# Optimization experiments

Hardware: AMD Instinct MI355X
Metric: run time of the kernel (lower is better)

The kernel has to match this reference:

```python
import jax, jax.numpy as jnp
import numpy as np

N, FIN = 4096, 128
HEADS = [8, 1]
FEATS = [64, 64]
NEG_SLOPE = 0.2
EDGE_P = 0.01  # edge density for the synthetic graph


def _init_w(key, shape, fan_in, fan_out):
    # VarianceScaling(1.0, 'fan_avg', 'uniform')
    limit = jnp.sqrt(3.0 / ((fan_in + fan_out) / 2.0))
    return jax.random.uniform(key, shape, jnp.float32, -limit, limit)


def setup_inputs() -> dict:
    key = jax.random.key(0)
    ks = jax.random.split(key, 12)
    x = jax.random.normal(ks[0], (N, FIN), jnp.float32)
    # additive connectivity mask: 0 on edges (incl. self-loops), -1e9 elsewhere
    adj = jax.random.bernoulli(ks[1], EDGE_P, (N, N))
    adj = adj | jnp.eye(N, dtype=bool)
    mask = jnp.where(adj, 0.0, -1e9).astype(jnp.float32)

    fin0, out0 = FIN, HEADS[0] * FEATS[0]
    fin1, out1 = out0, HEADS[1] * FEATS[1]
    W0 = _init_w(ks[2], (fin0, out0), fin0, out0)
    b0 = jnp.zeros((out0,), jnp.float32)
    a_src0 = _init_w(ks[3], (1, HEADS[0], FEATS[0]), 1, HEADS[0] * FEATS[0])
    a_tgt0 = _init_w(ks[4], (1, HEADS[0], FEATS[0]), 1, HEADS[0] * FEATS[0])
    W1 = _init_w(ks[5], (fin1, out1), fin1, out1)
    b1 = jnp.zeros((out1,), jnp.float32)
    a_src1 = _init_w(ks[6], (1, HEADS[1], FEATS[1]), 1, HEADS[1] * FEATS[1])
    a_tgt1 = _init_w(ks[7], (1, HEADS[1], FEATS[1]), 1, HEADS[1] * FEATS[1])
    return {
        "node_features": x, "connectivity_mask": mask,
        "W0": W0, "b0": b0, "a_src0": a_src0, "a_tgt0": a_tgt0,
        "W1": W1, "b1": b1, "a_src1": a_src1, "a_tgt1": a_tgt1,
    }


def _gat_layer(x, mask, W, b, a_src, a_tgt, num_heads, num_features):
    # (N, FIN) @ (FIN, H*F) -> (N, H, F)
    proj = (x @ W + b).reshape(-1, num_heads, num_features)
    s_src = jnp.sum(proj * a_src, axis=-1)  # (N, H)
    s_tgt = jnp.sum(proj * a_tgt, axis=-1)  # (N, H)
    # (H, N, 1) + (H, 1, N) -> (H, N, N)
    scores = s_src.T[:, :, None] + s_tgt.T[:, None, :]
    scores = jax.nn.leaky_relu(scores, negative_slope=NEG_SLOPE)
    att = jax.nn.softmax(scores + mask[None, :, :], axis=-1)  # (H, N, N)
    out = jnp.einsum('hnm,mhf->nhf', att, proj)  # (N, H, F)
    return out.reshape(-1, num_heads * num_features)


def reference(node_features, connectivity_mask, W0, b0, a_src0, a_tgt0,
              W1, b1, a_src1, a_tgt1):
    h = _gat_layer(node_features, connectivity_mask, W0, b0, a_src0, a_tgt0,
                   HEADS[0], FEATS[0])
    h = _gat_layer(h, connectivity_mask, W1, b1, a_src1, a_tgt1,
                   HEADS[1], FEATS[1])
    return h  # (N, HEADS[1]*FEATS[1])
```

## Files before the change

### kernel.cpp

```cpp
#include <hip/hip_runtime.h>
#include <hip/hip_bf16.h>

#define NNODES 4096
#define CAP 256


__global__ __launch_bounds__(256) void phase1_kernel(
    const float* __restrict__ mask, int* __restrict__ deg,
    unsigned short* __restrict__ cols, const float* __restrict__ x,
    const float* __restrict__ W0, const float* __restrict__ b0,
    const float* __restrict__ a_src0, const float* __restrict__ a_tgt0,
    const float* __restrict__ W1, float* __restrict__ Ph,
    float* __restrict__ ssrc0, float* __restrict__ stgt0) {
  __shared__ float smem[6144];
  const int t = threadIdx.x;
  if (blockIdx.x >= 1024) {
    const int n = blockIdx.x - 1024;
    const int lane = t & 63, wid = t >> 6;
    int* wsum = (int*)smem;
    const float4* row = (const float4*)(mask + (size_t)n * NNODES);
    float4 v[4];
    int cnt = 0;
#pragma unroll
    for (int j = 0; j < 4; ++j) {
      v[j] = row[t + 256 * j];
      cnt += (v[j].x == 0.0f) + (v[j].y == 0.0f) + (v[j].z == 0.0f) +
             (v[j].w == 0.0f);
    }
    int xs = cnt;
#pragma unroll
    for (int o = 1; o < 64; o <<= 1) {
      int y = __shfl_up(xs, o);
      if (lane >= o) xs += y;
    }
    if (lane == 63) wsum[wid] = xs;
    __syncthreads();
    int base = 0;
    for (int w = 0; w < wid; ++w) base += wsum[w];
    int off = base + xs - cnt;
    if (t == 0) {
      int total = wsum[0] + wsum[1] + wsum[2] + wsum[3];
      deg[n] = total < CAP ? total : CAP;
    }
    unsigned short* dst = cols + (size_t)n * CAP;
#pragma unroll
    for (int j = 0; j < 4; ++j) {
      const int c0 = (t + 256 * j) * 4;
      float fv[4] = {v[j].x, v[j].y, v[j].z, v[j].w};
#pragma unroll
      for (int k = 0; k < 4; ++k) {
        if (fv[k] == 0.0f) {
          if (off < CAP) dst[off] = (unsigned short)(c0 + k);
          ++off;
        }
      }
    }
  } else {
    float(*As)[36] = (float(*)[36])smem;
    float(*Ws)[64] = (float(*)[64])(smem + 1152);
    const int bx = blockIdx.x;
    const int brow = (bx & 127) * 32;
    const int head = bx >> 7;
    const int bcol = head * 64;
    const int tx = t & 15, ty = t >> 4;
    const int ar = t >> 3, ak = (t & 7) * 4;
    float acc[2][4] = {};
    for (int c = 0; c < 4; ++c) {
      const int k0 = c * 32;
      *(float4*)&As[ar][ak] =
          *(const float4*)&x[(size_t)(brow + ar) * 128 + k0 + ak];
#pragma unroll
      for (int q = 0; q < 2; ++q) {
        int i = t + q * 256;
        int k = i >> 4, c4 = (i & 15) * 4;
        *(float4*)&Ws[k][c4] =
            *(const float4*)&W0[(size_t)(k0 + k) * 512 + bcol + c4];
      }
      __syncthreads();
#pragma unroll 2
      for (int kk = 0; kk < 32; kk += 4) {
        float4 a0 = *(const float4*)&As[ty * 2 + 0][kk];
        float4 a1 = *(const float4*)&As[ty * 2 + 1][kk];
#pragma unroll
        for (int j = 0; j < 4; ++j) {
          float4 w = *(const float4*)&Ws[kk + j][tx * 4];
          float av0 = ((const float*)&a0)[j];
          float av1 = ((const float*)&a1)[j];
          acc[0][0] = fmaf(av0, w.x, acc[0][0]);
          acc[0][1] = fmaf(av0, w.y, acc[0][1]);
          acc[0][2] = fmaf(av0, w.z, acc[0][2]);
          acc[0][3] = fmaf(av0, w.w, acc[0][3]);
          acc[1][0] = fmaf(av1, w.x, acc[1][0]);
          acc[1][1] = fmaf(av1, w.y, acc[1][1]);
          acc[1][2] = fmaf(av1, w.z, acc[1][2]);
          acc[1][3] = fmaf(av1, w.w, acc[1][3]);
        }
      }
      __syncthreads();
    }
    float(*tile)[64] = (float(*)[64])smem;
    float(*W1s)[64] = (float(*)[64])(smem + 2048);
    const float4 bv = *(const float4*)&b0[bcol + tx * 4];
    const float4 as = *(const float4*)&a_src0[head * 64 + tx * 4];
    const float4 at = *(const float4*)&a_tgt0[head * 64 + tx * 4];
#pragma unroll
    for (int r = 0; r < 2; ++r) {
      float4 o;
      o.x = acc[r][0] + bv.x; o.y = acc[r][1] + bv.y;
      o.z = acc[r][2] + bv.z; o.w = acc[r][3] + bv.w;
      const int rowl = ty * 2 + r;
      *(float4*)&tile[rowl][tx * 4] = o;
      float ps = o.x * as.x + o.y * as.y + o.z * as.z + o.w * as.w;
      float pt = o.x * at.x + o.y * at.y + o.z * at.z + o.w * at.w;
#pragma unroll
      for (int m = 8; m; m >>= 1) {
        ps += __shfl_xor(ps, m);
        pt += __shfl_xor(pt, m);
      }
      if (tx == 0) {
        const size_t node = brow + rowl;
        ssrc0[node * 8 + head] = ps;
        stgt0[node * 8 + head] = pt;
      }
    }
    for (int i = t; i < 1024; i += 256) {
      const int k = i >> 4, c4 = (i & 15) * 4;
      *(float4*)&W1s[k][c4] =
          *(const float4*)&W1[(size_t)(head * 64 + k) * 64 + c4];
    }
    __syncthreads();
    float acc2[2][4] = {};
#pragma unroll 4
    for (int k = 0; k < 64; ++k) {
      const float4 w4 = *(const float4*)&W1s[k][tx * 4];
      const float a0 = tile[ty * 2 + 0][k];
      const float a1 = tile[ty * 2 + 1][k];
      acc2[0][0] = fmaf(a0, w4.x, acc2[0][0]);
      acc2[0][1] = fmaf(a0, w4.y, acc2[0][1]);
      acc2[0][2] = fmaf(a0, w4.z, acc2[0][2]);
      acc2[0][3] = fmaf(a0, w4.w, acc2[0][3]);
      acc2[1][0] = fmaf(a1, w4.x, acc2[1][0]);
      acc2[1][1] = fmaf(a1, w4.y, acc2[1][1]);
      acc2[1][2] = fmaf(a1, w4.z, acc2[1][2]);
      acc2[1][3] = fmaf(a1, w4.w, acc2[1][3]);
    }
#pragma unroll
    for (int r = 0; r < 2; ++r) {
      float4 o;
      o.x = acc2[r][0]; o.y = acc2[r][1]; o.z = acc2[r][2]; o.w = acc2[r][3];
      *(float4*)&Ph[(size_t)(brow + ty * 2 + r) * 512 + head * 64 + tx * 4] = o;
    }
  }
}

__global__ __launch_bounds__(128) void attnP_kernel(
    const float* __restrict__ Ph, const float* __restrict__ ssrc0,
    const float* __restrict__ stgt0, const int* __restrict__ deg,
    const unsigned short* __restrict__ cols, float* __restrict__ part) {
  const int b = blockIdx.x;
  const int fh = (b & 7) >> 2;
  const int n = ((b >> 3) << 2) + (b & 3);
  const int t = threadIdx.x;
  const int lane = t & 63, wid = t >> 6;
  __shared__ int sm_[CAP];
  __shared__ float sw[CAP * 5];
  __shared__ float sinv[4];
  __shared__ float4 buf[16];
  const int d = deg[n];
  for (int i = t; i < d; i += 128) sm_[i] = cols[(size_t)n * CAP + i];
  __syncthreads();
  const int hbase = fh * 4;
  for (int i = t; i < d * 4; i += 128) {
    const int e = i >> 2, h = i & 3;
    float s = ssrc0[n * 8 + hbase + h] + stgt0[sm_[e] * 8 + hbase + h];
    sw[e * 5 + h] = s >= 0.f ? s : 0.2f * s;
  }
  __syncthreads();
  for (int h = wid; h < 4; h += 2) {
    float mx = -1e30f;
    for (int e = lane; e < d; e += 64) mx = fmaxf(mx, sw[e * 5 + h]);
#pragma unroll
    for (int o = 32; o; o >>= 1) mx = fmaxf(mx, __shfl_xor(mx, o));
    float sum = 0.f;
    for (int e = lane; e < d; e += 64) {
      float w = __expf(sw[e * 5 + h] - mx);
      sw[e * 5 + h] = w;
      sum += w;
    }
#pragma unroll
    for (int o = 32; o; o >>= 1) sum += __shfl_xor(sum, o);
    if (lane == 0) sinv[h] = 1.0f / sum;
  }
  __syncthreads();
  const int grp = t >> 6;
  const int hl = lane >> 4;
  float4 a0 = make_float4(0.f, 0.f, 0.f, 0.f), a1 = a0;
  int e = grp;
  for (; e + 2 < d; e += 4) {
    const int m0 = sm_[e], m1 = sm_[e + 2];
    const float w0 = sw[e * 5 + hl], w1 = sw[(e + 2) * 5 + hl];
    const float4 p0 =
        *(const float4*)&Ph[(size_t)m0 * 512 + fh * 256 + lane * 4];
    const float4 p1 =
        *(const float4*)&Ph[(size_t)m1 * 512 + fh * 256 + lane * 4];
    a0.x = fmaf(w0, p0.x, a0.x); a0.y = fmaf(w0, p0.y, a0.y);
    a0.z = fmaf(w0, p0.z, a0.z); a0.w = fmaf(w0, p0.w, a0.w);
    a1.x = fmaf(w1, p1.x, a1.x); a1.y = fmaf(w1, p1.y, a1.y);
    a1.z = fmaf(w1, p1.z, a1.z); a1.w = fmaf(w1, p1.w, a1.w);
  }
  for (; e < d; e += 2) {
    const float w = sw[e * 5 + hl];
    const float4 pv =
        *(const float4*)&Ph[(size_t)sm_[e] * 512 + fh * 256 + lane * 4];
    a0.x = fmaf(w, pv.x, a0.x); a0.y = fmaf(w, pv.y, a0.y);
    a0.z = fmaf(w, pv.z, a0.z); a0.w = fmaf(w, pv.w, a0.w);
  }
  const float s = sinv[hl];
  float4 acc;
  acc.x = (a0.x + a1.x) * s;
  acc.y = (a0.y + a1.y) * s;
  acc.z = (a0.z + a1.z) * s;
  acc.w = (a0.w + a1.w) * s;
#pragma unroll
  for (int o = 16; o <= 32; o <<= 1) {
    acc.x += __shfl_xor(acc.x, o);
    acc.y += __shfl_xor(acc.y, o);
    acc.z += __shfl_xor(acc.z, o);
    acc.w += __shfl_xor(acc.w, o);
  }
  if (grp == 1 && lane < 16) buf[lane] = acc;
  __syncthreads();
  if (grp == 0 && lane < 16) {
    const float4 o2 = buf[lane];
    float4 o;
    o.x = acc.x + o2.x; o.y = acc.y + o2.y;
    o.z = acc.z + o2.z; o.w = acc.w + o2.w;
    *(float4*)&part[(size_t)fh * (NNODES * 64) + (size_t)n * 64 + lane * 4] = o;
  }
}

__global__ __launch_bounds__(256) void finalize_scores1_kernel(
    const float* __restrict__ part, const float* __restrict__ bias,
    const float* __restrict__ a_src1, const float* __restrict__ a_tgt1,
    float* __restrict__ proj1, float* __restrict__ ssrc1,
    float* __restrict__ stgt1) {
  const int i = blockIdx.x * 256 + threadIdx.x;
  const float4* p = (const float4*)part;
  float4 a = p[i], b = p[i + 65536];
  const int f4 = i & 15;
  const float4 bb = *(const float4*)&bias[f4 * 4];
  float4 r;
  r.x = a.x + b.x + bb.x;
  r.y = a.y + b.y + bb.y;
  r.z = a.z + b.z + bb.z;
  r.w = a.w + b.w + bb.w;
  ((float4*)proj1)[i] = r;
  const float4 as = *(const float4*)&a_src1[f4 * 4];
  const float4 at = *(const float4*)&a_tgt1[f4 * 4];
  float ps = r.x * as.x + r.y * as.y + r.z * as.z + r.w * as.w;
  float pt = r.x * at.x + r.y * at.y + r.z * at.z + r.w * at.w;
#pragma unroll
  for (int m = 8; m; m >>= 1) {
    ps += __shfl_xor(ps, m);
    pt += __shfl_xor(pt, m);
  }
  if (f4 == 0) {
    const int node = i >> 4;
    ssrc1[node] = ps;
    stgt1[node] = pt;
  }
}

__global__ void attn1_kernel(
    const float* __restrict__ proj, const float* __restrict__ s_src,
    const float* __restrict__ s_tgt, const int* __restrict__ deg,
    const unsigned short* __restrict__ cols, float* __restrict__ out) {
  const int n = blockIdx.x;
  const int tid = threadIdx.x;
  __shared__ int sm_[CAP];
  __shared__ float sw[CAP];
  const int d = deg[n];
  for (int i = tid; i < d; i += 64) sm_[i] = cols[(size_t)n * CAP + i];
  __syncthreads();
  const float ssn = s_src[n];
  for (int i = tid; i < d; i += 64) {
    float s = ssn + s_tgt[sm_[i]];
    sw[i] = s >= 0.f ? s : 0.2f * s;
  }
  __syncthreads();
  float mx = -1e30f;
  for (int e = tid; e < d; e += 64) mx = fmaxf(mx, sw[e]);
#pragma unroll
  for (int o = 32; o; o >>= 1) mx = fmaxf(mx, __shfl_xor(mx, o));
  float sum = 0.f;
  for (int e = tid; e < d; e += 64) {
    float w = __expf(sw[e] - mx);
    sw[e] = w;
    sum += w;
  }
#pragma unroll
  for (int o = 32; o; o >>= 1) sum += __shfl_xor(sum, o);
  const float sinv = 1.0f / sum;
  __syncthreads();
  const int f4 = tid & 15, grp = tid >> 4;
  float4 acc = make_float4(0.f, 0.f, 0.f, 0.f);
  for (int e = grp; e < d; e += 4) {
    const float w = sw[e];
    const float4 pv = *(const float4*)&proj[(size_t)sm_[e] * 64 + f4 * 4];
    acc.x = fmaf(w, pv.x, acc.x);
    acc.y = fmaf(w, pv.y, acc.y);
    acc.z = fmaf(w, pv.z, acc.z);
    acc.w = fmaf(w, pv.w, acc.w);
  }
#pragma unroll
  for (int o = 16; o <= 32; o <<= 1) {
    acc.x += __shfl_xor(acc.x, o);
    acc.y += __shfl_xor(acc.y, o);
    acc.z += __shfl_xor(acc.z, o);
    acc.w += __shfl_xor(acc.w, o);
  }
  if (grp == 0) {
    acc.x *= sinv; acc.y *= sinv; acc.z *= sinv; acc.w *= sinv;
    *(float4*)&out[(size_t)n * 64 + f4 * 4] = acc;
  }
}

extern "C" void kernel_launch(void* const* d_in, const int* in_sizes, int n_in,
                              void* d_out, int out_size, void* d_ws, size_t ws_size,
                              hipStream_t stream) {
  const float* x      = (const float*)d_in[0];
  const float* mask   = (const float*)d_in[1];
  const float* W0     = (const float*)d_in[2];
  const float* b0     = (const float*)d_in[3];
  const float* a_src0 = (const float*)d_in[4];
  const float* a_tgt0 = (const float*)d_in[5];
  const float* W1     = (const float*)d_in[6];
  const float* b1     = (const float*)d_in[7];
  const float* a_src1 = (const float*)d_in[8];
  const float* a_tgt1 = (const float*)d_in[9];
  float* out = (float*)d_out;

  float* ws    = (float*)d_ws;
  float* Ph    = ws;
  float* part  = Ph + NNODES * 512;
  float* proj1 = part + 2 * NNODES * 64;
  float* ssrc0 = proj1 + NNODES * 64;
  float* stgt0 = ssrc0 + NNODES * 8;
  float* ssrc1 = stgt0 + NNODES * 8;
  float* stgt1 = ssrc1 + NNODES;
  int* deg = (int*)(stgt1 + NNODES);
  unsigned short* cols = (unsigned short*)(deg + NNODES);

  phase1_kernel<<<NNODES + 1024, 256, 0, stream>>>(
      mask, deg, cols, x, W0, b0, a_src0, a_tgt0, W1, Ph, ssrc0, stgt0);
  attnP_kernel<<<NNODES * 2, 128, 0, stream>>>(Ph, ssrc0, stgt0, deg, cols, part);
  finalize_scores1_kernel<<<256, 256, 0, stream>>>(part, b1, a_src1, a_tgt1,
                                                   proj1, ssrc1, stgt1);
  attn1_kernel<<<NNODES, 64, 0, stream>>>(proj1, ssrc1, stgt1, deg, cols, out);
}
```

Before: 59.48 us.

## Split layer-0 aggregation into four head-pair blocks of one wavefront each

The layer-0 attention aggregation is re-partitioned so each 64-thread block handles two heads (a quarter of the 512 features) of one node, instead of 128-thread blocks handling four heads. This removes the cross-wavefront shared-memory reduction and its extra barriers, and raises the number of blocks to four per node. In exchange, each block recomputes the neighbor index load, and the finalize kernel now sums four partial buffers instead of two, adding workspace traffic.

```diff
diff --git a/kernel.cpp b/kernel.cpp
--- a/kernel.cpp
+++ b/kernel.cpp
@@ -153,69 +153,72 @@
   }
 }
 
-__global__ __launch_bounds__(128) void attnP_kernel(
+__global__ __launch_bounds__(64) void attnQ_kernel(
     const float* __restrict__ Ph, const float* __restrict__ ssrc0,
     const float* __restrict__ stgt0, const int* __restrict__ deg,
     const unsigned short* __restrict__ cols, float* __restrict__ part) {
   const int b = blockIdx.x;
-  const int fh = (b & 7) >> 2;
-  const int n = ((b >> 3) << 2) + (b & 3);
-  const int t = threadIdx.x;
-  const int lane = t & 63, wid = t >> 6;
+  const int xg = b & 7;
+  const int fq = xg >> 1;
+  const int n = ((b >> 3) << 1) | (xg & 1);
+  const int lane = threadIdx.x;
   __shared__ int sm_[CAP];
-  __shared__ float sw[CAP * 5];
-  __shared__ float sinv[4];
-  __shared__ float4 buf[16];
+  __shared__ float sw[CAP * 3];
   const int d = deg[n];
-  for (int i = t; i < d; i += 128) sm_[i] = cols[(size_t)n * CAP + i];
-  __syncthreads();
-  const int hbase = fh * 4;
-  for (int i = t; i < d * 4; i += 128) {
-    const int e = i >> 2, h = i & 3;
-    float s = ssrc0[n * 8 + hbase + h] + stgt0[sm_[e] * 8 + hbase + h];
-    sw[e * 5 + h] = s >= 0.f ? s : 0.2f * s;
-  }
-  __syncthreads();
-  for (int h = wid; h < 4; h += 2) {
+  for (int i = lane; i < d; i += 64) sm_[i] = cols[(size_t)n * CAP + i];
+  __syncthreads();
+  const int hbase = fq * 2;
+  const float ss0 = ssrc0[n * 8 + hbase + 0];
+  const float ss1 = ssrc0[n * 8 + hbase + 1];
+  for (int i = lane; i < d * 2; i += 64) {
+    const int e = i >> 1, h = i & 1;
+    float s = (h ? ss1 : ss0) + stgt0[sm_[e] * 8 + hbase + h];
+    sw[e * 3 + h] = s >= 0.f ? s : 0.2f * s;
+  }
+  __syncthreads();
+  float sinv[2];
+#pragma unroll
+  for (int h = 0; h < 2; ++h) {
     float mx = -1e30f;
-    for (int e = lane; e < d; e += 64) mx = fmaxf(mx, sw[e * 5 + h]);
+    for (int e = lane; e < d; e += 64) mx = fmaxf(mx, sw[e * 3 + h]);
 #pragma unroll
     for (int o = 32; o; o >>= 1) mx = fmaxf(mx, __shfl_xor(mx, o));
     float sum = 0.f;
     for (int e = lane; e < d; e += 64) {
-      float w = __expf(sw[e * 5 + h] - mx);
-      sw[e * 5 + h] = w;
+      float w = __expf(sw[e * 3 + h] - mx);
+      sw[e * 3 + h] = w;
       sum += w;
     }
 #pragma unroll
     for (int o = 32; o; o >>= 1) sum += __shfl_xor(sum, o);
-    if (lane == 0) sinv[h] = 1.0f / sum;
-  }
-  __syncthreads();
-  const int grp = t >> 6;
-  const int hl = lane >> 4;
+    sinv[h] = 1.0f / sum;
+  }
+  __syncthreads();
+  const int grp = lane >> 5;
+  const int l32 = lane & 31;
+  const int hl = l32 >> 4;
+  const float s = sinv[hl];
   float4 a0 = make_float4(0.f, 0.f, 0.f, 0.f), a1 = a0;
   int e = grp;
   for (; e + 2 < d; e += 4) {
     const int m0 = sm_[e], m1 = sm_[e + 2];
-    const float w0 = sw[e * 5 + hl], w1 = sw[(e + 2) * 5 + hl];
+    const float w0 = sw[e * 3 + hl], w1 = sw[(e + 2) * 3 + hl];
     const float4 p0 =
-        *(const float4*)&Ph[(size_t)m0 * 512 + fh * 256 + lane * 4];
+        *(const float4*)&Ph[(size_t)m0 * 512 + fq * 128 + l32 * 4];
     const float4 p1 =
-        *(const float4*)&Ph[(size_t)m1 * 512 + fh * 256 + lane * 4];
+        *(const float4*)&Ph[(size_t)m1 * 512 + fq * 128 + l32 * 4];
     a0.x = fmaf(w0, p0.x, a0.x); a0.y = fmaf(w0, p0.y, a0.y);
     a0.z = fmaf(w0, p0.z, a0.z); a0.w = fmaf(w0, p0.w, a0.w);
     a1.x = fmaf(w1, p1.x, a1.x); a1.y = fmaf(w1, p1.y, a1.y);
     a1.z = fmaf(w1, p1.z, a1.z); a1.w = fmaf(w1, p1.w, a1.w);
   }
   for (; e < d; e += 2) {
-    const float w = sw[e * 5 + hl];
+    const float w = sw[e * 3 + hl];
     const float4 pv =
-        *(const float4*)&Ph[(size_t)sm_[e] * 512 + fh * 256 + lane * 4];
+        *(const float4*)&Ph[(size_t)sm_[e] * 512 + fq * 128 + l32 * 4];
     a0.x = fmaf(w, pv.x, a0.x); a0.y = fmaf(w, pv.y, a0.y);
     a0.z = fmaf(w, pv.z, a0.z); a0.w = fmaf(w, pv.w, a0.w);
   }
-  const float s = sinv[hl];
   float4 acc;
   acc.x = (a0.x + a1.x) * s;
   acc.y = (a0.y + a1.y) * s;
@@ -228,14 +231,9 @@
     acc.z += __shfl_xor(acc.z, o);
     acc.w += __shfl_xor(acc.w, o);
   }
-  if (grp == 1 && lane < 16) buf[lane] = acc;
-  __syncthreads();
-  if (grp == 0 && lane < 16) {
-    const float4 o2 = buf[lane];
-    float4 o;
-    o.x = acc.x + o2.x; o.y = acc.y + o2.y;
-    o.z = acc.z + o2.z; o.w = acc.w + o2.w;
-    *(float4*)&part[(size_t)fh * (NNODES * 64) + (size_t)n * 64 + lane * 4] = o;
+  if (lane < 16) {
+    *(float4*)&part[(size_t)fq * (NNODES * 64) + (size_t)n * 64 + lane * 4] =
+        acc;
   }
 }
 
@@ -246,14 +244,14 @@
     float* __restrict__ stgt1) {
   const int i = blockIdx.x * 256 + threadIdx.x;
   const float4* p = (const float4*)part;
-  float4 a = p[i], b = p[i + 65536];
+  float4 a = p[i], b = p[i + 65536], c = p[i + 131072], dd = p[i + 196608];
   const int f4 = i & 15;
   const float4 bb = *(const float4*)&bias[f4 * 4];
   float4 r;
-  r.x = a.x + b.x + bb.x;
-  r.y = a.y + b.y + bb.y;
-  r.z = a.z + b.z + bb.z;
-  r.w = a.w + b.w + bb.w;
+  r.x = a.x + b.x + c.x + dd.x + bb.x;
+  r.y = a.y + b.y + c.y + dd.y + bb.y;
+  r.z = a.z + b.z + c.z + dd.z + bb.z;
+  r.w = a.w + b.w + c.w + dd.w + bb.w;
   ((float4*)proj1)[i] = r;
   const float4 as = *(const float4*)&a_src1[f4 * 4];
   const float4 at = *(const float4*)&a_tgt1[f4 * 4];
@@ -343,7 +341,7 @@
   float* ws    = (float*)d_ws;
   float* Ph    = ws;
   float* part  = Ph + NNODES * 512;
-  float* proj1 = part + 2 * NNODES * 64;
+  float* proj1 = part + 4 * NNODES * 64;
   float* ssrc0 = proj1 + NNODES * 64;
   float* stgt0 = ssrc0 + NNODES * 8;
   float* ssrc1 = stgt0 + NNODES * 8;
@@ -353,7 +351,7 @@
 
   phase1_kernel<<<NNODES + 1024, 256, 0, stream>>>(
       mask, deg, cols, x, W0, b0, a_src0, a_tgt0, W1, Ph, ssrc0, stgt0);
-  attnP_kernel<<<NNODES * 2, 128, 0, stream>>>(Ph, ssrc0, stgt0, deg, cols, part);
+  attnQ_kernel<<<NNODES * 4, 64, 0, stream>>>(Ph, ssrc0, stgt0, deg, cols, part);
   finalize_scores1_kernel<<<256, 256, 0, stream>>>(part, b1, a_src1, a_tgt1,
                                                    proj1, ssrc1, stgt1);
   attn1_kernel<<<NNODES, 64, 0, stream>>>(proj1, ssrc1, stgt1, deg, cols, out);
```

Result: faster. 56.80 us (-4.5%).
